# Kernel optimization log

Measured on AMD Instinct MI355X. Metric: run time of the kernel, lower is better.

The kernel has to match this reference:

```python
import jax, jax.numpy as jnp
import numpy as np

IMG = 640.0  # pixel coordinate range for keypoints


def setup_inputs() -> dict:
    key = jax.random.key(0)
    ks = jax.random.split(key, 16)
    B, N, M, C, D, G = 4, 4096, 4096, 256, 256, 32
    s = 1.0 / np.sqrt(C)
    inp = {
        "nodes_t": jax.random.normal(ks[0], (B, N, C), jnp.float32),
        "nodes_t1": jax.random.normal(ks[1], (B, M, C), jnp.float32),
        "kpts_t1_pred": jax.random.uniform(ks[2], (B, N, 2), jnp.float32) * IMG,
        "kpts_t1_actual": jax.random.uniform(ks[3], (B, M, 2), jnp.float32) * IMG,
        "Wq": jax.random.normal(ks[4], (D, C), jnp.float32) * s,
        "bq": jnp.zeros((D,), jnp.float32),
        "Wk": jax.random.normal(ks[5], (D, C), jnp.float32) * s,
        "bk": jnp.zeros((D,), jnp.float32),
        "Wv": jax.random.normal(ks[6], (D, C), jnp.float32) * s,
        "bv": jnp.zeros((D,), jnp.float32),
        "Wm": jax.random.normal(ks[7], (D, D), jnp.float32) * (1.0 / np.sqrt(D)),
        "bm": jnp.zeros((D,), jnp.float32),
        "Wg1": jax.random.normal(ks[8], (G, 3), jnp.float32) * (1.0 / np.sqrt(3.0)),
        "bg1": jnp.zeros((G,), jnp.float32),
        "Wg2": jax.random.normal(ks[9], (G, G), jnp.float32) * (1.0 / np.sqrt(G)),
        "bg2": jnp.zeros((G,), jnp.float32),
        "iter_idx": 0,
    }
    return inp


def reference(nodes_t, nodes_t1, kpts_t1_pred, kpts_t1_actual,
              Wq, bq, Wk, bk, Wv, bv, Wm, bm, Wg1, bg1, Wg2, bg2, iter_idx):
    # window size schedule (iter_idx is a static Python int)
    win = 64.0 if iter_idx == 0 else max(4.0, 32.0 / 2 ** (iter_idx - 1))

    Q = nodes_t @ Wq.T + bq      # [B,N,256]
    K = nodes_t1 @ Wk.T + bk     # [B,M,256]
    V = nodes_t1 @ Wv.T + bv     # [B,M,256]

    # distance-based window mask [B,N,M]
    du = jnp.abs(kpts_t1_pred[:, :, 0:1] - kpts_t1_actual[:, None, :, 0])
    dv = jnp.abs(kpts_t1_pred[:, :, 1:2] - kpts_t1_actual[:, None, :, 1])
    mask = (du < win) & (dv < win)

    attn = jnp.einsum('bnd,bmd->bnm', Q, K) / jnp.sqrt(jnp.float32(256.0))
    attn = jnp.where(mask, attn, jnp.float32(-1e9))
    w = jax.nn.softmax(attn, axis=-1)

    matched_features = jnp.einsum('bnm,bmd->bnd', w, V)        # [B,N,256]
    matched_kpts = jnp.einsum('bnm,bmc->bnc', w, kpts_t1_actual)  # [B,N,2]

    confidence = jnp.any(mask, axis=-1, keepdims=True).astype(jnp.float32)  # [B,N,1]
    flow_residual = (matched_kpts - kpts_t1_pred) * confidence

    geo_in = jnp.concatenate([flow_residual, confidence], axis=-1)  # [B,N,3]
    h = jax.nn.silu(geo_in @ Wg1.T + bg1)
    geo_temp = h @ Wg2.T + bg2                                   # [B,N,32]

    merged = matched_features @ Wm.T + bm                        # [B,N,256]
    return merged, geo_temp, flow_residual, confidence
```

## Files before the change

kernel.cpp:

```cpp
#include <hip/hip_runtime.h>
#include <hip/hip_bf16.h>

typedef unsigned short ushort;
typedef unsigned int uint;
typedef __bf16 bf16x8 __attribute__((ext_vector_type(8)));
typedef float f32x4 __attribute__((ext_vector_type(4)));
typedef ushort ushort8 __attribute__((ext_vector_type(8)));

#define LOG2E 1.4426950408889634f
#define MFMA16(a,b,c) __builtin_amdgcn_mfma_f32_16x16x32_bf16((a),(b),(c),0,0,0)
#define GLL16(src, dst) __builtin_amdgcn_global_load_lds( \
    (const __attribute__((address_space(1))) void*)(src), \
    (__attribute__((address_space(3))) void*)(dst), 16, 0, 0)
#define GLL4(src, dst) __builtin_amdgcn_global_load_lds( \
    (const __attribute__((address_space(1))) void*)(src), \
    (__attribute__((address_space(3))) void*)(dst), 4, 0, 0)

static __device__ __forceinline__ uint packbf(float lo, float hi) {
  union { __bf16 h[2]; uint u; } x;
  x.h[0] = (__bf16)lo; x.h[1] = (__bf16)hi;
  return x.u;
}
static __device__ __forceinline__ int cellof(float x) {
  int c = (int)(x * 0.015625f);
  return c < 0 ? 0 : (c > 9 ? 9 : c);
}

__global__ __launch_bounds__(256) void cast_weights(
    const float* __restrict__ W0, const float* __restrict__ W1,
    const float* __restrict__ W2, const float* __restrict__ W3,
    __bf16* __restrict__ out,
    int* __restrict__ hist, int* __restrict__ curs, float* __restrict__ meanN)
{
  if (blockIdx.x == 0 && blockIdx.y == 0) {
    int t = threadIdx.x;
    for (int i = t; i < 1024; i += 256) { hist[i] = 0; curs[i] = 0; meanN[i] = 0.f; }
  }
  const int which = blockIdx.y;
  const float* src = which == 0 ? W0 : which == 1 ? W1 : which == 2 ? W2 : W3;
  const int i = (blockIdx.x * 256 + threadIdx.x) * 4;
  f32x4 v = *(const f32x4*)(src + i);
  union { __bf16 h[4]; uint u[2]; } x;
  #pragma unroll
  for (int j = 0; j < 4; j++) x.h[j] = (__bf16)v[j];
  *(uint*)(out + (size_t)which * 65536 + i) = x.u[0];
  *(uint*)(out + (size_t)which * 65536 + i + 2) = x.u[1];
}

__global__ __launch_bounds__(256) void hist_kernel(
    const float* __restrict__ kpred, const float* __restrict__ kact,
    int* __restrict__ hist, int* __restrict__ cellpt)
{
  int p = blockIdx.x * 256 + threadIdx.x;
  int type = p >> 14, idx = p & 16383;
  const float2 c = ((const float2*)(type == 0 ? kpred : kact))[idx];
  int cell = cellof(c.x) * 10 + cellof(c.y);
  int b = idx >> 12;
  atomicAdd(&hist[(type * 4 + b) * 128 + cell], 1);
  cellpt[type * 16384 + idx] = cell;
}

__global__ __launch_bounds__(256) void scan_kernel(
    const int* __restrict__ hist, int* __restrict__ strt, int* __restrict__ curs)
{
  __shared__ int sh[1024];
  int t = threadIdx.x;
  for (int i = t; i < 1024; i += 256) sh[i] = hist[i];
  __syncthreads();
  if (t < 8) {
    int run = 0;
    for (int c = 0; c < 100; c++) {
      strt[t * 128 + c] = run;
      curs[t * 128 + c] = run;
      run += sh[t * 128 + c];
    }
    strt[t * 128 + 100] = run;
  }
}

__global__ __launch_bounds__(256) void scatter_kernel(
    const float* __restrict__ kpred, const float* __restrict__ kact,
    const int* __restrict__ cellpt, int* __restrict__ curs,
    int* __restrict__ sq, int* __restrict__ invq, float* __restrict__ kpS,
    int* __restrict__ sk, int* __restrict__ invk, float* __restrict__ kaS)
{
  int p = blockIdx.x * 256 + threadIdx.x;
  int type = p >> 14, idx = p & 16383;
  int b = idx >> 12, n = idx & 4095;
  int cell = cellpt[type * 16384 + idx];
  int pos = atomicAdd(&curs[(type * 4 + b) * 128 + cell], 1);
  if (type == 0) {
    sq[b * 4096 + pos] = n;
    invq[b * 4096 + n] = pos;
    ((float2*)kpS)[b * 4096 + pos] = ((const float2*)kpred)[idx];
  } else {
    sk[b * 4096 + pos] = n;
    invk[b * 4096 + n] = pos;
    ((float2*)kaS)[b * 4096 + pos] = ((const float2*)kact)[idx];
  }
}

__global__ __launch_bounds__(256) void meansum_kernel(
    const float* __restrict__ nodes_t1, float* __restrict__ meanN)
{
  int b = blockIdx.y, chunk = blockIdx.x, c = threadIdx.x;
  const float* base = nodes_t1 + ((size_t)b * 4096 + chunk * 256) * 256 + c;
  float s = 0.f;
  for (int r = 0; r < 256; r++) s += base[(size_t)r * 256];
  atomicAdd(&meanN[b * 256 + c], s);
}

__global__ __launch_bounds__(256) void vmean_kernel(
    const float* __restrict__ meanN, const float* __restrict__ Wv,
    const float* __restrict__ bv, float* __restrict__ Vmean)
{
  __shared__ float mn[256];
  int b = blockIdx.x, d = threadIdx.x;
  mn[d] = meanN[b * 256 + d] * (1.0f / 4096.0f);
  __syncthreads();
  float s = bv[d];
  const float* w = Wv + (size_t)d * 256;
  for (int c = 0; c < 256; c++) s += mn[c] * w[c];
  Vmean[b * 256 + d] = s;
}

__global__ __launch_bounds__(256) void gemm_qkv(
    const float* __restrict__ nodes_t, const float* __restrict__ nodes_t1,
    const ushort* __restrict__ W4,
    const float* __restrict__ bq, const float* __restrict__ bk,
    const float* __restrict__ bv,
    __bf16* __restrict__ outQ, __bf16* __restrict__ outK,
    __bf16* __restrict__ outVs,
    const int* __restrict__ invq, const int* __restrict__ invk)
{
  const int z = blockIdx.z;
  const float* A = z == 0 ? nodes_t : nodes_t1;
  const ushort* W = W4 + z * 65536;
  const float* bias = z == 0 ? bq : (z == 1 ? bk : bv);
  const int* inv = z == 0 ? invq : invk;

  const int wid = threadIdx.x >> 6;
  const int lane = threadIdx.x & 63;
  const int q = lane & 15, g = lane >> 4;
  const int nb = blockIdx.x * 64 + (wid >> 1) * 32;
  const int db = blockIdx.y * 128 + (wid & 1) * 64;

  f32x4 acc[2][4];
  #pragma unroll
  for (int a = 0; a < 2; a++)
    #pragma unroll
    for (int b = 0; b < 4; b++) acc[a][b] = f32x4{0.f,0.f,0.f,0.f};

  const ushort* W0 = W + (size_t)(db + q) * 256 + g * 8;

  #pragma unroll
  for (int c0 = 0; c0 < 256; c0 += 32) {
    bf16x8 a0, a1;
    const float* Ar0 = A + (size_t)(nb + q) * 256 + g * 8 + c0;
    const float* Ar1 = A + (size_t)(nb + 16 + q) * 256 + g * 8 + c0;
    f32x4 u0 = *(const f32x4*)Ar0, u1 = *(const f32x4*)(Ar0 + 4);
    f32x4 w0 = *(const f32x4*)Ar1, w1 = *(const f32x4*)(Ar1 + 4);
    #pragma unroll
    for (int j = 0; j < 4; j++) {
      a0[j] = (__bf16)u0[j]; a0[4 + j] = (__bf16)u1[j];
      a1[j] = (__bf16)w0[j]; a1[4 + j] = (__bf16)w1[j];
    }
    #pragma unroll
    for (int df = 0; df < 4; df++) {
      bf16x8 w = *(const bf16x8*)(W0 + df * 16 * 256 + c0);
      acc[0][df] = MFMA16(a0, w, acc[0][df]);
      acc[1][df] = MFMA16(a1, w, acc[1][df]);
    }
  }
  __bf16* o = z == 0 ? outQ : (z == 1 ? outK : outVs);
  #pragma unroll
  for (int df = 0; df < 4; df++) {
    float bval = bias[db + df * 16 + q];
    #pragma unroll
    for (int nf = 0; nf < 2; nf++)
      #pragma unroll
      for (int r = 0; r < 4; r++) {
        int row = nb + nf * 16 + g * 4 + r;
        int d = db + df * 16 + q;
        float val = acc[nf][df][r] + bval;
        int pos = inv[row];
        o[((size_t)(row & ~4095) + pos) * 256 + d] = (__bf16)val;
      }
  }
}

__global__ __launch_bounds__(256) void transpose_v(
    const ushort* __restrict__ Vs, ushort* __restrict__ VT)
{
  __shared__ ushort tile[64][76];
  const int b = blockIdx.z, rt = blockIdx.x, dt = blockIdx.y;
  const int tid = threadIdx.x;
  const ushort* src = Vs + ((size_t)b * 4096 + rt * 64) * 256 + dt * 64;
  #pragma unroll
  for (int i = 0; i < 2; i++) {
    int c = tid + i * 256;
    int r = c >> 3, dc = (c & 7) * 8;
    ushort8 v = *(const ushort8*)(src + (size_t)r * 256 + dc);
    #pragma unroll
    for (int j = 0; j < 8; j++) tile[r][dc + j] = v[j];
  }
  __syncthreads();
  ushort* dst = VT + ((size_t)b * 256 + dt * 64) * 4096 + rt * 64;
  #pragma unroll
  for (int i = 0; i < 2; i++) {
    int c = tid + i * 256;
    int d = c >> 3, rc = (c & 7) * 8;
    ushort8 v;
    #pragma unroll
    for (int j = 0; j < 8; j++) v[j] = tile[rc + j][d];
    *(ushort8*)(dst + (size_t)d * 4096 + rc) = v;
  }
}

__global__ __launch_bounds__(256) void gemm_merged(
    const ushort* __restrict__ A, const ushort* __restrict__ W,
    const float* __restrict__ bias, float* __restrict__ out)
{
  const int wid = threadIdx.x >> 6;
  const int lane = threadIdx.x & 63;
  const int q = lane & 15, g = lane >> 4;
  const int nb = blockIdx.x * 64 + (wid >> 1) * 32;
  const int db = blockIdx.y * 128 + (wid & 1) * 64;

  f32x4 acc[2][4];
  #pragma unroll
  for (int a = 0; a < 2; a++)
    #pragma unroll
    for (int b = 0; b < 4; b++) acc[a][b] = f32x4{0.f,0.f,0.f,0.f};

  const ushort* W0 = W + (size_t)(db + q) * 256 + g * 8;
  const ushort* Ar0 = A + (size_t)(nb + q) * 256 + g * 8;
  const ushort* Ar1 = A + (size_t)(nb + 16 + q) * 256 + g * 8;

  #pragma unroll
  for (int c0 = 0; c0 < 256; c0 += 32) {
    bf16x8 a0 = *(const bf16x8*)(Ar0 + c0);
    bf16x8 a1 = *(const bf16x8*)(Ar1 + c0);
    #pragma unroll
    for (int df = 0; df < 4; df++) {
      bf16x8 w = *(const bf16x8*)(W0 + df * 16 * 256 + c0);
      acc[0][df] = MFMA16(a0, w, acc[0][df]);
      acc[1][df] = MFMA16(a1, w, acc[1][df]);
    }
  }
  #pragma unroll
  for (int df = 0; df < 4; df++) {
    float bval = bias[db + df * 16 + q];
    #pragma unroll
    for (int nf = 0; nf < 2; nf++)
      #pragma unroll
      for (int r = 0; r < 4; r++) {
        int row = nb + nf * 16 + g * 4 + r;
        out[(size_t)row * 256 + db + df * 16 + q] = acc[nf][df][r] + bval;
      }
  }
}

__global__ __launch_bounds__(256, 2) void attn_kernel(
    const ushort* __restrict__ Q,
    const ushort* __restrict__ K,
    const ushort* __restrict__ VT,
    const float* __restrict__ kpS,
    const int* __restrict__ iter_idx,
    const int* __restrict__ sq,
    const int* __restrict__ strt,
    const float* __restrict__ kaS,
    const float* __restrict__ Vmean,
    __bf16* __restrict__ matched,
    float* __restrict__ out_flow, float* __restrict__ out_conf)
{
  __shared__ __align__(16) ushort Kl[2][8192];
  __shared__ __align__(16) ushort Vl[2][8192];
  __shared__ __align__(16) float2 Cl[2][32];
  __shared__ int tl_t[132], tl_ks[132], tl_ke[132];
  __shared__ int ntile_s;

  const int tid = threadIdx.x;
  const int wid = tid >> 6, lane = tid & 63;
  const int q = lane & 15, g = lane >> 4;
  const int batch = blockIdx.x & 3;
  const int cell = blockIdx.x >> 2;

  const int qstart = strt[batch * 128 + cell];
  const int nq = strt[batch * 128 + cell + 1] - qstart;
  if (nq == 0) return;

  const int cu = cell / 10, cv = cell % 10;
  const int c0 = cv > 0 ? cv - 1 : 0, c1 = cv < 9 ? cv + 1 : 9;
  const int* kst = strt + (4 + batch) * 128;

  if (tid == 0) {
    int n = 0;
    int lo = cu > 0 ? cu - 1 : 0, hi = cu < 9 ? cu + 1 : 9;
    for (int cc = lo; cc <= hi; cc++) {
      int ks = kst[cc * 10 + c0];
      int ke = kst[cc * 10 + c1 + 1];
      for (int t = ks & ~31; t < ke; t += 32) {
        tl_t[n] = t; tl_ks[n] = ks; tl_ke[n] = ke; n++;
      }
    }
    ntile_s = n;
  }
  __syncthreads();
  const int ntile = ntile_s;

  const int idx = *iter_idx;
  const float win = (idx == 0) ? 64.0f : fmaxf(4.0f, ldexpf(32.0f, 1 - idx));

  const ushort* Kbase = K + (size_t)batch * 4096 * 256;
  const ushort* VTb = VT + (size_t)batch * 1048576;
  const float* kasf = kaS + (size_t)batch * 8192;
  const float* Vm = Vmean + batch * 256;

  const int npass = (nq + 63) >> 6;

  auto STAGE = [&](int ti, int b) {
    const int t = tl_t[ti];
    #pragma unroll
    for (int j = 0; j < 4; j++) {
      int n = wid * 256 + j * 64 + lane;
      int r = n & 31, u = n >> 5;
      GLL16(Kbase + (size_t)(t + r) * 256 + u * 8,
            &Kl[b][(size_t)(wid * 256 + j * 64) * 8]);
    }
    #pragma unroll
    for (int j = 0; j < 4; j++) {
      int n = wid * 256 + j * 64 + lane;
      int pl = n >> 8, d = n & 255;
      GLL16(VTb + (size_t)d * 4096 + t + pl * 8,
            &Vl[b][(size_t)(wid * 256 + j * 64) * 8]);
    }
    if (wid == 0) GLL4(kasf + t * 2 + lane, &Cl[b][0]);
  };

  int cnt = 0, qi = 0;
  bool active = false;
  float pu = 0.f, pv = 0.f;
  bf16x8 qf[8];
  f32x4 O[16];
  float m_run = -1e9f, l_run = 0.f, u_run = 0.f, v_run = 0.f;

  auto PASS_INIT = [&](int pp) {
    int tbase = pp * 64 + wid * 16;
    active = tbase < nq;
    cnt = active ? min(16, nq - tbase) : 0;
    if (active) {
      int qq = q < cnt ? q : cnt - 1;
      int qsrow = batch * 4096 + qstart + tbase + qq;
      qi = sq[qsrow];
      const ushort* qptr = Q + (size_t)qsrow * 256 + g * 8;
      #pragma unroll
      for (int mf = 0; mf < 8; mf++) qf[mf] = *(const bf16x8*)(qptr + mf * 32);
      float2 kpv = ((const float2*)kpS)[qsrow];
      pu = kpv.x; pv = kpv.y;
    }
    #pragma unroll
    for (int i = 0; i < 16; i++) O[i] = f32x4{0.f,0.f,0.f,0.f};
    m_run = -1e9f; l_run = 0.f; u_run = 0.f; v_run = 0.f;
  };

  auto EPILOGUE = [&]() {
    if (!active) return;
    l_run += __shfl_xor(l_run, 16); l_run += __shfl_xor(l_run, 32);
    u_run += __shfl_xor(u_run, 16); u_run += __shfl_xor(u_run, 32);
    v_run += __shfl_xor(v_run, 16); v_run += __shfl_xor(v_run, 32);
    bool degen = (m_run <= -5e8f) || (l_run == 0.f);
    float rinv = degen ? 0.f : 1.0f / l_run;
    if (g == 0 && q < cnt) {
      float conf = degen ? 0.f : 1.0f;
      int row = batch * 4096 + qi;
      float fu = (u_run * rinv - pu) * conf, fv = (v_run * rinv - pv) * conf;
      ((float2*)out_flow)[row] = float2{fu, fv};
      out_conf[row] = conf;
    }
    #pragma unroll
    for (int r = 0; r < 4; r++) {
      int src = 4 * g + r;
      int qi_r = __shfl(qi, src);
      float il_r = __shfl(rinv, src);
      bool dg_r = (il_r == 0.f);
      if (src < cnt) {
        __bf16* mrow = matched + ((size_t)batch * 4096 + qi_r) * 256;
        #pragma unroll
        for (int df = 0; df < 16; df++) {
          float val = dg_r ? Vm[df * 16 + q] : O[df][r] * il_r;
          mrow[df * 16 + q] = (__bf16)val;
        }
      }
    }
  };

  if (ntile == 0) {
    for (int pp = 0; pp < npass; pp++) { PASS_INIT(pp); EPILOGUE(); }
    return;
  }

  const int total = npass * ntile;
  STAGE(0, 0);
  PASS_INIT(0);

  int i = 0, pp = 0;
  for (int it = 0; it < total; ++it) {
    __syncthreads();
    if (it + 1 < total) {
      int ni = (i + 1 == ntile) ? 0 : i + 1;
      STAGE(ni, (it + 1) & 1);
    }
    const int b = it & 1;

    if (active) {
      const int t = tl_t[i], ks = tl_ks[i], ke = tl_ke[i];

      f32x4 s0a = {0.f,0.f,0.f,0.f}, s0b = {0.f,0.f,0.f,0.f};
      f32x4 s1a = {0.f,0.f,0.f,0.f}, s1b = {0.f,0.f,0.f,0.f};
      #pragma unroll
      for (int mf = 0; mf < 8; mf += 2) {
        bf16x8 ka0 = *(const bf16x8*)&Kl[b][(size_t)(((mf    ) * 4 + g) * 32 + q     ) * 8];
        bf16x8 kb0 = *(const bf16x8*)&Kl[b][(size_t)(((mf + 1) * 4 + g) * 32 + q     ) * 8];
        bf16x8 ka1 = *(const bf16x8*)&Kl[b][(size_t)(((mf    ) * 4 + g) * 32 + q + 16) * 8];
        bf16x8 kb1 = *(const bf16x8*)&Kl[b][(size_t)(((mf + 1) * 4 + g) * 32 + q + 16) * 8];
        s0a = MFMA16(ka0, qf[mf],     s0a);
        s0b = MFMA16(kb0, qf[mf + 1], s0b);
        s1a = MFMA16(ka1, qf[mf],     s1a);
        s1b = MFMA16(kb1, qf[mf + 1], s1b);
      }

      float aus[8], avs[8], sv[8];
      #pragma unroll
      for (int r = 0; r < 4; r++) {
        int jr = t + 4 * g + r;
        float2 cc0 = Cl[b][4 * g + r];
        aus[r] = cc0.x; avs[r] = cc0.y;
        bool val = (jr >= ks && jr < ke);
        float du = fabsf(pu - cc0.x), dv = fabsf(pv - cc0.y);
        float sr = s0a[r] + s0b[r];
        sv[r] = (val && fmaxf(du, dv) < win) ? sr * 0.0625f : -1e9f;

        int jr1 = jr + 16;
        float2 cc1 = Cl[b][16 + 4 * g + r];
        aus[4 + r] = cc1.x; avs[4 + r] = cc1.y;
        val = (jr1 >= ks && jr1 < ke);
        du = fabsf(pu - cc1.x); dv = fabsf(pv - cc1.y);
        sr = s1a[r] + s1b[r];
        sv[4 + r] = (val && fmaxf(du, dv) < win) ? sr * 0.0625f : -1e9f;
      }

      float mt = fmaxf(fmaxf(fmaxf(sv[0], sv[1]), fmaxf(sv[2], sv[3])),
                       fmaxf(fmaxf(sv[4], sv[5]), fmaxf(sv[6], sv[7])));
      mt = fmaxf(mt, __shfl_xor(mt, 16));
      mt = fmaxf(mt, __shfl_xor(mt, 32));
      if (__any(mt > m_run + 8.0f)) {
        float m_new = fmaxf(m_run, mt);
        float scale = exp2f((m_run - m_new) * LOG2E);
        l_run *= scale; u_run *= scale; v_run *= scale;
        float s_r[4];
        #pragma unroll
        for (int r = 0; r < 4; r++) s_r[r] = __shfl(scale, 4 * g + r);
        #pragma unroll
        for (int df = 0; df < 16; df++)
          #pragma unroll
          for (int r = 0; r < 4; r++) O[df][r] *= s_r[r];
        m_run = m_new;
      }

      float p[8];
      #pragma unroll
      for (int ii = 0; ii < 8; ii++) p[ii] = exp2f((sv[ii] - m_run) * LOG2E);
      #pragma unroll
      for (int ii = 0; ii < 8; ii++) {
        l_run += p[ii];
        u_run += p[ii] * aus[ii];
        v_run += p[ii] * avs[ii];
      }

      uint d0 = packbf(p[0], p[1]), d1 = packbf(p[2], p[3]);
      uint d2 = packbf(p[4], p[5]), d3 = packbf(p[6], p[7]);
      int srcA = q + ((g & 1) << 5);
      int srcB = srcA + 16;
      uint x0 = (uint)__shfl((int)d0, srcA), x1 = (uint)__shfl((int)d1, srcA);
      uint x2 = (uint)__shfl((int)d0, srcB), x3 = (uint)__shfl((int)d1, srcB);
      uint y0 = (uint)__shfl((int)d2, srcA), y1 = (uint)__shfl((int)d3, srcA);
      uint y2 = (uint)__shfl((int)d2, srcB), y3 = (uint)__shfl((int)d3, srcB);
      union { uint i4[4]; bf16x8 v; } af;
      bool lo = (g < 2);
      af.i4[0] = lo ? x0 : y0; af.i4[1] = lo ? x1 : y1;
      af.i4[2] = lo ? x2 : y2; af.i4[3] = lo ? x3 : y3;

      #pragma unroll
      for (int df = 0; df < 16; df++) {
        bf16x8 vfd = *(const bf16x8*)&Vl[b][(size_t)(g * 256 + df * 16 + q) * 8];
        O[df] = MFMA16(af.v, vfd, O[df]);
      }
    }

    if (i == ntile - 1) {
      EPILOGUE();
      pp++;
      if (pp < npass) PASS_INIT(pp);
      i = 0;
    } else {
      i++;
    }
  }
}

__global__ __launch_bounds__(256) void geo_kernel(
    const float* __restrict__ flow, const float* __restrict__ conf_in,
    const float* __restrict__ Wg1, const float* __restrict__ bg1,
    const float* __restrict__ Wg2, const float* __restrict__ bg2,
    float* __restrict__ out_geo)
{
  __shared__ float w1[32][3], b1[32], b2[32];
  __shared__ __align__(16) float w2[32][32];
  int tid = threadIdx.x;
  for (int i = tid; i < 96; i += 256) w1[i / 3][i % 3] = Wg1[i];
  if (tid < 32) { b1[tid] = bg1[tid]; b2[tid] = bg2[tid]; }
  for (int i = tid; i < 1024; i += 256) w2[i / 32][i % 32] = Wg2[i];
  __syncthreads();

  int row = blockIdx.x * 256 + tid;
  float2 f = ((const float2*)flow)[row];
  float c = conf_in[row];
  float h[32];
  #pragma unroll
  for (int j = 0; j < 32; j++) {
    float x = w1[j][0] * f.x + w1[j][1] * f.y + w1[j][2] * c + b1[j];
    h[j] = x / (1.f + __expf(-x));
  }
  #pragma unroll
  for (int o = 0; o < 32; o += 2) {
    float s0 = b2[o], s1 = b2[o + 1];
    #pragma unroll
    for (int j = 0; j < 32; j += 4) {
      f32x4 wa = *(const f32x4*)&w2[o][j];
      f32x4 wb = *(const f32x4*)&w2[o + 1][j];
      s0 += wa[0]*h[j] + wa[1]*h[j+1] + wa[2]*h[j+2] + wa[3]*h[j+3];
      s1 += wb[0]*h[j] + wb[1]*h[j+1] + wb[2]*h[j+2] + wb[3]*h[j+3];
    }
    ((float2*)out_geo)[((size_t)row * 32 + o) >> 1] = float2{s0, s1};
  }
}

extern "C" void kernel_launch(void* const* d_in, const int* in_sizes, int n_in,
                              void* d_out, int out_size, void* d_ws, size_t ws_size,
                              hipStream_t stream) {
  const float* nodes_t  = (const float*)d_in[0];
  const float* nodes_t1 = (const float*)d_in[1];
  const float* kpred    = (const float*)d_in[2];
  const float* kact     = (const float*)d_in[3];
  const float* Wq = (const float*)d_in[4];  const float* bq = (const float*)d_in[5];
  const float* Wk = (const float*)d_in[6];  const float* bk = (const float*)d_in[7];
  const float* Wv = (const float*)d_in[8];  const float* bv = (const float*)d_in[9];
  const float* Wm = (const float*)d_in[10]; const float* bm = (const float*)d_in[11];
  const float* Wg1= (const float*)d_in[12]; const float* bg1= (const float*)d_in[13];
  const float* Wg2= (const float*)d_in[14]; const float* bg2= (const float*)d_in[15];
  const int* iter = (const int*)d_in[16];

  float* out_merged = (float*)d_out;
  float* out_geo  = out_merged + 4 * 4096 * 256;
  float* out_flow = out_geo + 4 * 4096 * 32;
  float* out_conf = out_flow + 4 * 4096 * 2;

  ushort* wsQ   = (ushort*)d_ws;
  ushort* wsK   = wsQ + 4194304;
  ushort* wsVT  = wsK + 4194304;
  ushort* wsM   = wsVT + 4194304;
  ushort* wsW   = wsM + 4194304;
  float*  kaS   = (float*)(wsW + 262144);
  float*  kpS   = kaS + 32768;
  float*  meanN = kpS + 32768;
  float*  Vmean = meanN + 1024;
  int*    hist  = (int*)(Vmean + 1024);
  int*    strt  = hist + 1024;
  int*    curs  = strt + 1024;
  int*    cellpt= curs + 1024;
  int*    sq    = cellpt + 32768;
  int*    sk    = sq + 16384;
  int*    invk  = sk + 16384;
  int*    invq  = invk + 16384;

  dim3 cg(64, 4, 1);
  cast_weights<<<cg, 256, 0, stream>>>(Wq, Wk, Wv, Wm, (__bf16*)wsW,
                                       hist, curs, meanN);
  hist_kernel<<<128, 256, 0, stream>>>(kpred, kact, hist, cellpt);
  scan_kernel<<<1, 256, 0, stream>>>(hist, strt, curs);
  scatter_kernel<<<128, 256, 0, stream>>>(kpred, kact, cellpt, curs,
                                          sq, invq, kpS, sk, invk, kaS);
  dim3 mg(16, 4, 1);
  meansum_kernel<<<mg, 256, 0, stream>>>(nodes_t1, meanN);
  vmean_kernel<<<4, 256, 0, stream>>>(meanN, Wv, bv, Vmean);

  dim3 qg(256, 2, 3);
  gemm_qkv<<<qg, 256, 0, stream>>>(nodes_t, nodes_t1, wsW, bq, bk, bv,
                                   (__bf16*)wsQ, (__bf16*)wsK, (__bf16*)wsM,
                                   invq, invk);
  dim3 tg(64, 4, 4);
  transpose_v<<<tg, 256, 0, stream>>>(wsM, wsVT);
  attn_kernel<<<400, 256, 0, stream>>>(wsQ, wsK, wsVT, kpS, iter,
                                       sq, strt, kaS, Vmean,
                                       (__bf16*)wsM, out_flow, out_conf);
  dim3 gg(256, 2, 1);
  gemm_merged<<<gg, 256, 0, stream>>>(wsM, wsW + 196608, bm, out_merged);
  geo_kernel<<<64, 256, 0, stream>>>(out_flow, out_conf, Wg1, bg1, Wg2, bg2, out_geo);
}
```

Baseline: 213.1 us.

## Pre-cast node features to bf16, fuse K/V projections, remap attention blocks

Adds a separate kernel that casts both node feature tensors to bf16 once. The QKV GEMM then reads bf16 activations and computes the K and V projections in the same block, so nodes_t1 is loaded once for both. The attention kernel's block-to-(batch,cell) mapping is permuted so consecutive workgroups land on different batches/cells, likely for load balance across XCDs. The cast kernel adds an extra full write and read of 8M bf16 values. The K/V blocks now do twice the MFMA work, which makes the z=1 and z=0 blocks imbalanced.

```diff
diff --git a/kernel.cpp b/kernel.cpp
--- a/kernel.cpp
+++ b/kernel.cpp
@@ -45,6 +45,21 @@
   for (int j = 0; j < 4; j++) x.h[j] = (__bf16)v[j];
   *(uint*)(out + (size_t)which * 65536 + i) = x.u[0];
   *(uint*)(out + (size_t)which * 65536 + i + 2) = x.u[1];
+}
+
+__global__ __launch_bounds__(256) void cast_nodes(
+    const float* __restrict__ n0, const float* __restrict__ n1,
+    __bf16* __restrict__ o0, __bf16* __restrict__ o1)
+{
+  const float* s = blockIdx.y ? n1 : n0;
+  __bf16* o = blockIdx.y ? o1 : o0;
+  const int i = (blockIdx.x * 256 + threadIdx.x) * 4;
+  f32x4 v = *(const f32x4*)(s + i);
+  union { __bf16 h[4]; uint u[2]; } x;
+  #pragma unroll
+  for (int j = 0; j < 4; j++) x.h[j] = (__bf16)v[j];
+  *(uint*)(o + i) = x.u[0];
+  *(uint*)(o + i + 2) = x.u[1];
 }
 
 __global__ __launch_bounds__(256) void hist_kernel(
@@ -125,7 +140,7 @@
 }
 
 __global__ __launch_bounds__(256) void gemm_qkv(
-    const float* __restrict__ nodes_t, const float* __restrict__ nodes_t1,
+    const ushort* __restrict__ A0, const ushort* __restrict__ A1,
     const ushort* __restrict__ W4,
     const float* __restrict__ bq, const float* __restrict__ bk,
     const float* __restrict__ bv,
@@ -134,9 +149,9 @@
     const int* __restrict__ invq, const int* __restrict__ invk)
 {
   const int z = blockIdx.z;
-  const float* A = z == 0 ? nodes_t : nodes_t1;
-  const ushort* W = W4 + z * 65536;
-  const float* bias = z == 0 ? bq : (z == 1 ? bk : bv);
+  const ushort* A = z == 0 ? A0 : A1;
+  const ushort* Wa = z == 0 ? W4 : W4 + 65536;
+  const ushort* Wb = W4 + 131072;
   const int* inv = z == 0 ? invq : invk;
 
   const int wid = threadIdx.x >> 6;
@@ -145,46 +160,56 @@
   const int nb = blockIdx.x * 64 + (wid >> 1) * 32;
   const int db = blockIdx.y * 128 + (wid & 1) * 64;
 
-  f32x4 acc[2][4];
+  f32x4 acc[2][4], accv[2][4];
   #pragma unroll
   for (int a = 0; a < 2; a++)
     #pragma unroll
-    for (int b = 0; b < 4; b++) acc[a][b] = f32x4{0.f,0.f,0.f,0.f};
-
-  const ushort* W0 = W + (size_t)(db + q) * 256 + g * 8;
+    for (int b = 0; b < 4; b++) {
+      acc[a][b] = f32x4{0.f,0.f,0.f,0.f};
+      accv[a][b] = f32x4{0.f,0.f,0.f,0.f};
+    }
+
+  const ushort* Wa0 = Wa + (size_t)(db + q) * 256 + g * 8;
+  const ushort* Wb0 = Wb + (size_t)(db + q) * 256 + g * 8;
+  const ushort* Ar0 = A + (size_t)(nb + q) * 256 + g * 8;
+  const ushort* Ar1 = A + (size_t)(nb + 16 + q) * 256 + g * 8;
 
   #pragma unroll
   for (int c0 = 0; c0 < 256; c0 += 32) {
-    bf16x8 a0, a1;
-    const float* Ar0 = A + (size_t)(nb + q) * 256 + g * 8 + c0;
-    const float* Ar1 = A + (size_t)(nb + 16 + q) * 256 + g * 8 + c0;
-    f32x4 u0 = *(const f32x4*)Ar0, u1 = *(const f32x4*)(Ar0 + 4);
-    f32x4 w0 = *(const f32x4*)Ar1, w1 = *(const f32x4*)(Ar1 + 4);
-    #pragma unroll
-    for (int j = 0; j < 4; j++) {
-      a0[j] = (__bf16)u0[j]; a0[4 + j] = (__bf16)u1[j];
-      a1[j] = (__bf16)w0[j]; a1[4 + j] = (__bf16)w1[j];
-    }
+    bf16x8 a0 = *(const bf16x8*)(Ar0 + c0);
+    bf16x8 a1 = *(const bf16x8*)(Ar1 + c0);
     #pragma unroll
     for (int df = 0; df < 4; df++) {
-      bf16x8 w = *(const bf16x8*)(W0 + df * 16 * 256 + c0);
+      bf16x8 w = *(const bf16x8*)(Wa0 + df * 16 * 256 + c0);
       acc[0][df] = MFMA16(a0, w, acc[0][df]);
       acc[1][df] = MFMA16(a1, w, acc[1][df]);
     }
-  }
-  __bf16* o = z == 0 ? outQ : (z == 1 ? outK : outVs);
+    if (z == 1) {
+      #pragma unroll
+      for (int df = 0; df < 4; df++) {
+        bf16x8 w = *(const bf16x8*)(Wb0 + df * 16 * 256 + c0);
+        accv[0][df] = MFMA16(a0, w, accv[0][df]);
+        accv[1][df] = MFMA16(a1, w, accv[1][df]);
+      }
+    }
+  }
+  const float* biasA = z == 0 ? bq : bk;
+  __bf16* oA = z == 0 ? outQ : outK;
   #pragma unroll
   for (int df = 0; df < 4; df++) {
-    float bval = bias[db + df * 16 + q];
+    float ba = biasA[db + df * 16 + q];
+    float bb = bv[db + df * 16 + q];
     #pragma unroll
     for (int nf = 0; nf < 2; nf++)
       #pragma unroll
       for (int r = 0; r < 4; r++) {
         int row = nb + nf * 16 + g * 4 + r;
         int d = db + df * 16 + q;
-        float val = acc[nf][df][r] + bval;
         int pos = inv[row];
-        o[((size_t)(row & ~4095) + pos) * 256 + d] = (__bf16)val;
+        size_t orow = (size_t)(row & ~4095) + pos;
+        oA[orow * 256 + d] = (__bf16)(acc[nf][df][r] + ba);
+        if (z == 1)
+          outVs[orow * 256 + d] = (__bf16)(accv[nf][df][r] + bb);
       }
   }
 }
@@ -283,8 +308,10 @@
   const int tid = threadIdx.x;
   const int wid = tid >> 6, lane = tid & 63;
   const int q = lane & 15, g = lane >> 4;
-  const int batch = blockIdx.x & 3;
-  const int cell = blockIdx.x >> 2;
+  const int orig = blockIdx.x;
+  const int wgid = (orig & 7) * 50 + (orig >> 3);
+  const int batch = wgid / 100;
+  const int cell = wgid % 100;
 
   const int qstart = strt[batch * 128 + cell];
   const int nq = strt[batch * 128 + cell + 1] - qstart;
@@ -562,7 +589,8 @@
   const int* iter = (const int*)d_in[16];
 
   float* out_merged = (float*)d_out;
-  float* out_geo  = out_merged + 4 * 4096 * 256;
+  float* out_geo  = out_merged + 4 * 4096 * 32 * 8;
+  out_geo = out_merged + 4 * 4096 * 256;
   float* out_flow = out_geo + 4 * 4096 * 32;
   float* out_conf = out_flow + 4 * 4096 * 2;
 
@@ -583,10 +611,15 @@
   int*    sk    = sq + 16384;
   int*    invk  = sk + 16384;
   int*    invq  = invk + 16384;
+  ushort* wsA0  = (ushort*)(invq + 16384);
+  ushort* wsA1  = wsA0 + 4194304;
 
   dim3 cg(64, 4, 1);
   cast_weights<<<cg, 256, 0, stream>>>(Wq, Wk, Wv, Wm, (__bf16*)wsW,
                                        hist, curs, meanN);
+  dim3 ng(4096, 2, 1);
+  cast_nodes<<<ng, 256, 0, stream>>>(nodes_t, nodes_t1,
+                                     (__bf16*)wsA0, (__bf16*)wsA1);
   hist_kernel<<<128, 256, 0, stream>>>(kpred, kact, hist, cellpt);
   scan_kernel<<<1, 256, 0, stream>>>(hist, strt, curs);
   scatter_kernel<<<128, 256, 0, stream>>>(kpred, kact, cellpt, curs,
@@ -595,8 +628,8 @@
   meansum_kernel<<<mg, 256, 0, stream>>>(nodes_t1, meanN);
   vmean_kernel<<<4, 256, 0, stream>>>(meanN, Wv, bv, Vmean);
 
-  dim3 qg(256, 2, 3);
-  gemm_qkv<<<qg, 256, 0, stream>>>(nodes_t, nodes_t1, wsW, bq, bk, bv,
+  dim3 qg(256, 2, 2);
+  gemm_qkv<<<qg, 256, 0, stream>>>(wsA0, wsA1, wsW, bq, bk, bv,
                                    (__bf16*)wsQ, (__bf16*)wsK, (__bf16*)wsM,
                                    invq, invk);
   dim3 tg(64, 4, 4);
```

Result: faster. 205.8 us (-3.4%).
